# Optimization experiments

Measured on AMD Instinct MI355X. Metric: run time of the kernel, lower is better.

## Reference

```python
import jax, jax.numpy as jnp
import numpy as np

B, S, D_IN, D_OUT = 4, 4096, 1024, 1024

def setup_inputs() -> dict:
    key = jax.random.key(0)
    kx, kq, kk, kv = jax.random.split(key, 4)
    x = jax.random.normal(kx, (B, S, D_IN), dtype=jnp.float32)
    # torch nn.Linear stores weight as [d_out, d_in]; y = x @ W.T
    Wq = jax.random.normal(kq, (D_OUT, D_IN), dtype=jnp.float32) * 0.02
    Wk = jax.random.normal(kk, (D_OUT, D_IN), dtype=jnp.float32) * 0.02
    Wv = jax.random.normal(kv, (D_OUT, D_IN), dtype=jnp.float32) * 0.02
    return {"x": x, "Wq": Wq, "Wk": Wk, "Wv": Wv}

def reference(x, Wq, Wk, Wv):
    b, n, _ = x.shape
    d_out = Wk.shape[0]
    q = jnp.einsum('bnd,od->bno', x, Wq)
    k = jnp.einsum('bnd,od->bno', x, Wk)
    v = jnp.einsum('bnd,od->bno', x, Wv)
    scores = jnp.einsum('bqo,bko->bqk', q, k)  # [B, S, S]
    causal = jnp.triu(jnp.ones((n, n), dtype=bool), k=1)
    scores = jnp.where(causal, -jnp.inf, scores)
    attn = jax.nn.softmax(scores / jnp.sqrt(jnp.float32(d_out)), axis=-1)
    # dropout p=0.0 -> identity
    return jnp.einsum('bqk,bko->bqo', attn, v)
```

## Files before the change

### kernel.cpp

```cpp
#include <hip/hip_runtime.h>


typedef unsigned short u16;
typedef unsigned int u32;
typedef __attribute__((ext_vector_type(8))) short bf16x8;
typedef __attribute__((ext_vector_type(4))) float f32x4;
typedef __attribute__((ext_vector_type(8))) unsigned short u16x8;

__device__ __forceinline__ u16 f2bf(float f) {
  union { float f; unsigned u; } v; v.f = f;
  unsigned r = v.u + 0x7FFFu + ((v.u >> 16) & 1u);
  return (u16)(r >> 16);
}
__device__ __forceinline__ float bf2f(u16 h) {
  union { unsigned u; float f; } v; v.u = ((unsigned)h) << 16;
  return v.f;
}
__device__ __forceinline__ f32x4 mfma16(bf16x8 a, bf16x8 b, f32x4 c) {
  return __builtin_amdgcn_mfma_f32_16x16x32_bf16(a, b, c, 0, 0, 0);
}
__device__ __forceinline__ void gld_lds16(const u16* g, u16* l) {
  __builtin_amdgcn_global_load_lds(
      (const __attribute__((address_space(1))) u32*)g,
      (__attribute__((address_space(3))) u32*)l, 16, 0, 0);
}
#define BAR() __builtin_amdgcn_s_barrier()
#define LGKM0() do { asm volatile("s_waitcnt lgkmcnt(0)" ::: "memory"); \
                     __builtin_amdgcn_sched_barrier(0); } while (0)
#define VMCNT2() asm volatile("s_waitcnt vmcnt(2)" ::: "memory")
#define VMCNT0() asm volatile("s_waitcnt vmcnt(0)" ::: "memory")

__global__ __launch_bounds__(256)
void cast_f32_bf16(const float* __restrict__ src, u16* __restrict__ dst, int n8) {
  int i = blockIdx.x * 256 + threadIdx.x;
  if (i >= n8) return;
  const float4* s4 = (const float4*)src;
  float4 a = s4[2*i], b = s4[2*i+1];
  u16x8 o;
  o[0]=f2bf(a.x); o[1]=f2bf(a.y); o[2]=f2bf(a.z); o[3]=f2bf(a.w);
  o[4]=f2bf(b.x); o[5]=f2bf(b.y); o[6]=f2bf(b.z); o[7]=f2bf(b.w);
  ((u16x8*)dst)[i] = o;
}

#define GEMM8_CORE(Abase, Bbase)                                              \
  auto stageA = [&](int bufi, int h, int t) {                                 \
    _Pragma("unroll")                                                         \
    for (int i = 0; i < 2; ++i) {                                             \
      int ci = i * 512 + tid;                                                 \
      int r  = ci >> 3;                                                       \
      int c  = (ci & 7) ^ (r & 7);                                            \
      gld_lds16(Abase + (size_t)(h * 128 + r) * 1024 + t * 64 + c * 8,        \
                &At[bufi][h][ci * 8]);                                        \
    }                                                                         \
  };                                                                          \
  auto stageB = [&](int bufi, int h, int t) {                                 \
    _Pragma("unroll")                                                         \
    for (int i = 0; i < 2; ++i) {                                             \
      int ci = i * 512 + tid;                                                 \
      int r  = ci >> 3;                                                       \
      int c  = (ci & 7) ^ (r & 7);                                            \
      gld_lds16(Bbase + (size_t)(h * 128 + r) * 1024 + t * 64 + c * 8,        \
                &Bt[bufi][h][ci * 8]);                                        \
    }                                                                         \
  };                                                                          \
  bf16x8 af[4][2], bfr[2][2];                                                 \
  auto readA = [&](int bufi, int mb) {                                        \
    _Pragma("unroll")                                                         \
    for (int m = 0; m < 4; ++m)                                               \
      _Pragma("unroll")                                                       \
      for (int dk = 0; dk < 2; ++dk) {                                        \
        int r  = (mb + m) * 16 + c16;                                         \
        int ch = dk * 4 + g;                                                  \
        af[m][dk] = *(const bf16x8*)&At[bufi][wr][r * 64 + ((ch ^ (r & 7)) * 8)]; \
      }                                                                       \
  };                                                                          \
  auto readB = [&](int bufi, int nb) {                                        \
    _Pragma("unroll")                                                         \
    for (int n = 0; n < 2; ++n)                                               \
      _Pragma("unroll")                                                       \
      for (int dk = 0; dk < 2; ++dk) {                                        \
        int r  = (wc & 1) * 64 + (nb + n) * 16 + c16;                         \
        int ch = dk * 4 + g;                                                  \
        bfr[n][dk] = *(const bf16x8*)&Bt[bufi][wc >> 1][r * 64 + ((ch ^ (r & 7)) * 8)]; \
      }                                                                       \
  };                                                                          \
  auto domfma = [&](int mb, int nb) {                                         \
    __builtin_amdgcn_s_setprio(1);                                            \
    _Pragma("unroll")                                                         \
    for (int dk = 0; dk < 2; ++dk)                                            \
      _Pragma("unroll")                                                       \
      for (int m = 0; m < 4; ++m)                                             \
        _Pragma("unroll")                                                     \
        for (int n = 0; n < 2; ++n)                                           \
          acc[mb + m][nb + n] = mfma16(af[m][dk], bfr[n][dk], acc[mb + m][nb + n]); \
    __builtin_amdgcn_s_setprio(0);                                            \
  };                                                                          \
                \
  stageB(0, 0, 0); stageB(0, 1, 0); stageA(0, 0, 0); stageA(0, 1, 0);         \
  stageB(1, 0, 1);                                                            \
  VMCNT2();                                                                   \
  BAR();                                                                      \
  for (int it = 0; it < 8; ++it) {                                            \
    const bool pf = (it < 7);                                                 \
    const int t1 = 2 * it + 1, t2 = 2 * it + 2, t3 = 2 * it + 3;              \
                                               \
    readA(0, 0); readB(0, 0);                                                 \
    stageB(1, 1, t1);                                                         \
    BAR(); LGKM0();                                                           \
    domfma(0, 0);                                                             \
    BAR();                                                                    \
                                                    \
    readA(0, 4);                                                              \
    stageA(1, 0, t1);                                                         \
    BAR(); LGKM0();                                                           \
    domfma(4, 0);                                                             \
    BAR();                                                                    \
                                                    \
    readB(0, 2);                                                              \
    stageA(1, 1, t1);                                                         \
    BAR(); LGKM0();                                                           \
    domfma(4, 2);                                                             \
    BAR();                                                                    \
                                    \
    readA(0, 0);                                                              \
    if (pf) stageB(0, 0, t2);                                                 \
    BAR(); LGKM0();                                                           \
    domfma(0, 2);                                                             \
    if (pf) { VMCNT2(); } else { VMCNT0(); }                                  \
    BAR();                                                                    \
                                                             \
    readA(1, 0); readB(1, 0);                                                 \
    if (pf) stageB(0, 1, t2);                                                 \
    BAR(); LGKM0();                                                           \
    domfma(0, 0);                                                             \
    BAR();                                                                    \
                                                                  \
    readA(1, 4);                                                              \
    if (pf) stageA(0, 0, t2);                                                 \
    BAR(); LGKM0();                                                           \
    domfma(4, 0);                                                             \
    BAR();                                                                    \
                                                                  \
    readB(1, 2);                                                              \
    if (pf) stageA(0, 1, t2);                                                 \
    BAR(); LGKM0();                                                           \
    domfma(4, 2);                                                             \
    BAR();                                                                    \
                                                  \
    readA(1, 0);                                                              \
    if (pf) stageB(1, 0, t3);                                                 \
    BAR(); LGKM0();                                                           \
    domfma(0, 2);                                                             \
    if (pf) { VMCNT2(); } else { VMCNT0(); }                                  \
    BAR();                                                                    \
  }

__global__ __launch_bounds__(512, 1)
void qkv_gemm(const u16* __restrict__ X, const u16* __restrict__ W,
              u16* __restrict__ Qo, u16* __restrict__ Ko, u16* __restrict__ VTo) {
  __shared__ __align__(16) u16 At[2][2][128 * 64];
  __shared__ __align__(16) u16 Bt[2][2][128 * 64];
  const int tid = threadIdx.x;
  const int w = tid >> 6, lane = tid & 63;
  const int g = lane >> 4, c16 = lane & 15;
  const int wr = w >> 2, wc = w & 3;
  const int M0 = blockIdx.x * 256;
  const int N0 = blockIdx.y * 256;
  const u16* Abase = X + (size_t)M0 * 1024;
  const u16* Bbase = W + (size_t)N0 * 1024;

  f32x4 acc[8][4] = {};
  GEMM8_CORE(Abase, Bbase);

  const int which = N0 >> 10;
  const int colbase = N0 & 1023;
#pragma unroll
  for (int m = 0; m < 8; ++m) {
#pragma unroll
    for (int n = 0; n < 4; ++n) {
#pragma unroll
      for (int r = 0; r < 4; ++r) {
        int gm  = M0 + wr * 128 + m * 16 + 4 * g + r;
        int col = colbase + wc * 64 + n * 16 + c16;
        u16 hv = f2bf(acc[m][n][r]);
        if (which == 0) {
          Qo[(size_t)gm * 1024 + col] = hv;
        } else if (which == 1) {
          Ko[(size_t)gm * 1024 + col] = hv;
        } else {
          int b = gm >> 12, s2 = gm & 4095;
          VTo[((size_t)((b << 10) + col)) * 4096 + s2] = hv;
        }
      }
    }
  }
}

__global__ __launch_bounds__(512, 1)
void sgemm_exp(const u16* __restrict__ Q, const u16* __restrict__ K,
               u16* __restrict__ Spack, float* __restrict__ lpart) {
  __shared__ __align__(16) u16 At[2][2][128 * 64];
  __shared__ __align__(16) u16 Bt[2][2][128 * 64];
  __shared__ float lsum[256][4];
  const int tid = threadIdx.x;
  const int w = tid >> 6, lane = tid & 63;
  const int g = lane >> 4, c16 = lane & 15;
  const int wr = w >> 2, wc = w & 3;
  const int b = blockIdx.y;

  int L = blockIdx.x, qt = 0;
  while ((qt + 1) * (qt + 2) / 2 <= L) ++qt;
  const int kt = L - qt * (qt + 1) / 2;

  const u16* Abase = Q + (size_t)b * 4096 * 1024 + (size_t)qt * 256 * 1024;
  const u16* Bbase = K + (size_t)b * 4096 * 1024 + (size_t)kt * 256 * 1024;

  f32x4 acc[8][4] = {};
  GEMM8_CORE(Abase, Bbase);

  const int qt128 = 2 * qt + wr;
  const int kt128 = 2 * kt + (wc >> 1);
  const bool exists = (kt128 <= qt128);
  u16* Sb = Spack + (((size_t)b * 528 + (size_t)(qt128 * (qt128 + 1)) / 2 + kt128) << 14);
  const int q0 = qt * 256, k0g = kt * 256;
  float psum[8][4];
#pragma unroll
  for (int m = 0; m < 8; ++m)
#pragma unroll
    for (int r = 0; r < 4; ++r) psum[m][r] = 0.f;
#pragma unroll
  for (int m = 0; m < 8; ++m) {
#pragma unroll
    for (int n = 0; n < 4; ++n) {
#pragma unroll
      for (int r = 0; r < 4; ++r) {
        int rl = wr * 128 + m * 16 + 4 * g + r;
        int cl = wc * 64 + n * 16 + c16;
        float s = acc[m][n][r] * 0.03125f;
        float p = (k0g + cl <= q0 + rl) ? __expf(s) : 0.f;
        u16 pb = f2bf(p);
        if (exists) Sb[(rl & 127) * 128 + (cl & 127)] = pb;
        psum[m][r] += bf2f(pb);
      }
    }
  }
#pragma unroll
  for (int m = 0; m < 8; ++m)
#pragma unroll
    for (int r = 0; r < 4; ++r) {
      float v = psum[m][r];
      v += __shfl_xor(v, 1, 64);
      v += __shfl_xor(v, 2, 64);
      v += __shfl_xor(v, 4, 64);
      v += __shfl_xor(v, 8, 64);
      psum[m][r] = v;
    }
  if (c16 == 0) {
#pragma unroll
    for (int m = 0; m < 8; ++m)
#pragma unroll
      for (int r = 0; r < 4; ++r)
        lsum[wr * 128 + m * 16 + 4 * g + r][wc] = psum[m][r];
  }
  __syncthreads();
  if (tid < 256) {
    float v = lsum[tid][0] + lsum[tid][1] + lsum[tid][2] + lsum[tid][3];
    lpart[((size_t)b * 4096 + q0 + tid) * 16 + kt] = v;
  }
}

__global__ __launch_bounds__(256)
void lreduce(const float* __restrict__ lpart, float* __restrict__ linv) {
  int row = blockIdx.x * 256 + threadIdx.x;
  int nt  = ((row & 4095) >> 8) + 1;
  const float* p = lpart + (size_t)row * 16;
  float s = 0.f;
  for (int i = 0; i < nt; ++i) s += p[i];
  linv[row] = 1.f / s;
}

__global__ __launch_bounds__(512)
void pv_gemm(const u16* __restrict__ Spack, const u16* __restrict__ VT,
             const u16* __restrict__ ztile, const float* __restrict__ linv,
             float* __restrict__ Out) {
  __shared__ __align__(16) u16 At[2][256 * 64];
  __shared__ __align__(16) u16 Bt[2][128 * 64];
  const int tid = threadIdx.x;
  const int w = tid >> 6, lane = tid & 63;
  const int g = lane >> 4, c16 = lane & 15;
  const int wm = w >> 1, wn = w & 1;
  const int pp = blockIdx.x;
  const int d0 = blockIdx.y;
  const int b  = blockIdx.z;

  const u16* Sp_b = Spack + (size_t)b * 528 * 16384;
  const u16* VTb  = VT + (size_t)b * 1024 * 4096;
  float* Ob = Out + (size_t)b * 4096 * 1024;

  for (int pass = 0; pass < 2; ++pass) {
    const int QT = pass == 0 ? pp : 15 - pp;
    const int M0 = QT * 256;
    const int nsteps = (QT + 1) * 4;
    const int tLo = 2 * QT;
    const size_t triLo = (size_t)(tLo * (tLo + 1)) / 2;
    const size_t triHi = (size_t)((tLo + 1) * (tLo + 2)) / 2;

    f32x4 acc[4][4] = {};

    auto stage = [&](int s, int tt) {
      const int kv0 = tt * 64;
      const int kt128 = tt >> 1;
      const int koff = (tt & 1) * 64;
      const u16* baseLo = (kt128 <= tLo) ? Sp_b + ((triLo + kt128) << 14) : ztile;
      const u16* baseHi = Sp_b + ((triHi + kt128) << 14);
#pragma unroll
      for (int i = 0; i < 4; ++i) {
        int ci = i * 512 + tid;
        int r = ci >> 3;
        int c = (ci & 7) ^ (r & 7);
        const u16* base = (i < 2) ? baseLo : baseHi;
        gld_lds16(base + (size_t)(r & 127) * 128 + koff + c * 8, &At[s][ci * 8]);
      }
#pragma unroll
      for (int i = 0; i < 2; ++i) {
        int ci = i * 512 + tid;
        int r = ci >> 3;
        int c = (ci & 7) ^ (r & 7);
        gld_lds16(VTb + (size_t)(d0 * 128 + r) * 4096 + kv0 + c * 8, &Bt[s][ci * 8]);
      }
    };
    auto compute = [&](int s) {
#pragma unroll
      for (int dk = 0; dk < 2; ++dk) {
        bf16x8 af2[4], bf2[4];
#pragma unroll
        for (int m = 0; m < 4; ++m) {
          int row = wm * 64 + m * 16 + c16;
          int ch = dk * 4 + g;
          af2[m] = *(const bf16x8*)&At[s][row * 64 + ((ch ^ (row & 7)) * 8)];
        }
#pragma unroll
        for (int n = 0; n < 4; ++n) {
          int row = wn * 64 + n * 16 + c16;
          int ch = dk * 4 + g;
          bf2[n] = *(const bf16x8*)&Bt[s][row * 64 + ((ch ^ (row & 7)) * 8)];
        }
#pragma unroll
        for (int m = 0; m < 4; ++m)
#pragma unroll
          for (int n = 0; n < 4; ++n)
            acc[m][n] = mfma16(af2[m], bf2[n], acc[m][n]);
      }
    };

    stage(0, 0);
    __syncthreads();
    int cur = 0;
    for (int t = 0; t < nsteps; ++t) {
      if (t + 1 < nsteps) stage(cur ^ 1, t + 1);
      compute(cur);
      __syncthreads();
      cur ^= 1;
    }

    const float* lb = linv + (size_t)b * 4096 + M0;
#pragma unroll
    for (int m = 0; m < 4; ++m) {
#pragma unroll
      for (int r = 0; r < 4; ++r) {
        int rl = wm * 64 + m * 16 + 4 * g + r;
        float li = lb[rl];
#pragma unroll
        for (int n = 0; n < 4; ++n) {
          int dcol = d0 * 128 + wn * 64 + n * 16 + c16;
          Ob[(size_t)(M0 + rl) * 1024 + dcol] = acc[m][n][r] * li;
        }
      }
    }
  }
}

__global__ __launch_bounds__(512, 2)
void attn_kernel(const u16* __restrict__ Q, const u16* __restrict__ K,
                 const u16* __restrict__ VT, float* __restrict__ Out) {
  __shared__ u16 kv_lds[32 * 1024];
  __shared__ float s_part[4][32][33];
  __shared__ u16 p_lds[32 * 40];
  __shared__ float l_lds[32];

  const int tid = threadIdx.x;
  const int w = tid >> 6, lane = tid & 63;
  const int g = lane >> 4, c16 = lane & 15;
  const int b  = blockIdx.x & 3;
  const int qb = 127 - (blockIdx.x >> 2);
  const int qs = qb * 32;
  const int kh = w & 1, dq = w >> 1;

  const u16* Qb  = Q  + (size_t)b * 4096 * 1024;
  const u16* Kb  = K  + (size_t)b * 4096 * 1024;
  const u16* VTb = VT + (size_t)b * 1024 * 4096;

  bf16x8 qfrag[2][8];
#pragma unroll
  for (int qh = 0; qh < 2; ++qh)
#pragma unroll
    for (int dk = 0; dk < 8; ++dk)
      qfrag[qh][dk] = *(const bf16x8*)(Qb + (size_t)(qs + qh * 16 + c16) * 1024
                                       + dq * 256 + dk * 32 + g * 8);

  f32x4 oacc[2][8] = {};
  if (tid < 32) l_lds[tid] = 0.f;

  const int qrow_p = tid >> 4;
  const int kk     = tid & 15;
  const int gq     = qs + qrow_p;

  for (int j = 0; j <= qb; ++j) {
    const int kv0 = j * 32;
    __syncthreads();
    uint4 rk[8];
#pragma unroll
    for (int i = 0; i < 8; ++i) {
      int ci = i * 512 + tid;
      int r  = ci >> 7;
      int c  = (ci & 127) ^ (r & 7);
      rk[i] = *(const uint4*)(Kb + (size_t)(kv0 + r) * 1024 + c * 8);
    }
#pragma unroll
    for (int i = 0; i < 8; ++i)
      *(uint4*)&kv_lds[(size_t)(i * 512 + tid) * 8] = rk[i];
    __syncthreads();
    f32x4 sacc[2] = {};
#pragma unroll
    for (int dk = 0; dk < 8; ++dk) {
      int kvrow = kh * 16 + c16;
      int ch    = dq * 32 + dk * 4 + g;
      bf16x8 kf = *(const bf16x8*)&kv_lds[kvrow * 1024 + ((ch ^ (kvrow & 7)) * 8)];
      sacc[0] = mfma16(qfrag[0][dk], kf, sacc[0]);
      sacc[1] = mfma16(qfrag[1][dk], kf, sacc[1]);
    }
#pragma unroll
    for (int qh = 0; qh < 2; ++qh)
#pragma unroll
      for (int r = 0; r < 4; ++r)
        s_part[dq][qh * 16 + 4 * g + r][kh * 16 + c16] = sacc[qh][r];
    __syncthreads();
    uint4 rv[8];
#pragma unroll
    for (int i = 0; i < 8; ++i) {
      int ci = i * 512 + tid;
      int d  = ((ci >> 6) << 4) + (ci & 15);
      int c  = (ci >> 4) & 3;
      rv[i] = *(const uint4*)(VTb + (size_t)d * 4096 + kv0 + c * 8);
    }
    {
      float psum = 0.f;
#pragma unroll
      for (int h = 0; h < 2; ++h) {
        int kcol = kk + h * 16;
        float s = s_part[0][qrow_p][kcol] + s_part[1][qrow_p][kcol]
                + s_part[2][qrow_p][kcol] + s_part[3][qrow_p][kcol];
        s *= 0.03125f;
        float p = (kv0 + kcol <= gq) ? __expf(s) : 0.f;
        u16 pb = f2bf(p);
        p_lds[qrow_p * 40 + kcol] = pb;
        psum += bf2f(pb);
      }
#pragma unroll
      for (int off = 1; off < 16; off <<= 1)
        psum += __shfl_xor(psum, off, 64);
      if (kk == 0) l_lds[qrow_p] += psum;
    }
#pragma unroll
    for (int i = 0; i < 8; ++i)
      *(uint4*)&kv_lds[(size_t)(i * 512 + tid) * 8] = rv[i];
    __syncthreads();
    bf16x8 pa0 = *(const bf16x8*)&p_lds[(0  + c16) * 40 + g * 8];
    bf16x8 pa1 = *(const bf16x8*)&p_lds[(16 + c16) * 40 + g * 8];
#pragma unroll
    for (int f = 0; f < 8; ++f) {
      int dcol = w * 128 + f * 16 + c16;
      int pos  = (dcol >> 4) * 64 + g * 16 + (dcol & 15);
      bf16x8 vf = *(const bf16x8*)&kv_lds[(size_t)pos * 8];
      oacc[0][f] = mfma16(pa0, vf, oacc[0][f]);
      oacc[1][f] = mfma16(pa1, vf, oacc[1][f]);
    }
  }

  float* Ob = Out + (size_t)b * 4096 * 1024;
#pragma unroll
  for (int qh = 0; qh < 2; ++qh) {
#pragma unroll
    for (int r = 0; r < 4; ++r) {
      int ql = qh * 16 + 4 * g + r;
      float linvv = 1.f / l_lds[ql];
#pragma unroll
      for (int f = 0; f < 8; ++f)
        Ob[(size_t)(qs + ql) * 1024 + w * 128 + f * 16 + c16] = oacc[qh][f][r] * linvv;
    }
  }
}

extern "C" void kernel_launch(void* const* d_in, const int* in_sizes, int n_in,
                              void* d_out, int out_size, void* d_ws, size_t ws_size,
                              hipStream_t stream) {
  const float* x  = (const float*)d_in[0];
  const float* Wq = (const float*)d_in[1];
  const float* Wk = (const float*)d_in[2];
  const float* Wv = (const float*)d_in[3];
  float* out = (float*)d_out;

  u16* ws    = (u16*)d_ws;
  u16* wWqkv = ws;
  u16* wX    = wWqkv + (size_t)3 * 1024 * 1024;
  u16* wQ    = wX + (size_t)16384 * 1024;
  u16* wK    = wQ + (size_t)16384 * 1024;
  u16* wVT   = wK + (size_t)16384 * 1024;
  u16* wSp   = wVT + (size_t)16384 * 1024;
  float* lpart = (float*)(ws + (size_t)104857600);
  float* linv  = (float*)(ws + (size_t)105906176);

  cast_f32_bf16<<<dim3(8192), 256, 0, stream>>>(x, wX, 16777216 / 8);
  cast_f32_bf16<<<dim3(512), 256, 0, stream>>>(Wq, wWqkv,                 1048576 / 8);
  cast_f32_bf16<<<dim3(512), 256, 0, stream>>>(Wk, wWqkv + 1048576,       1048576 / 8);
  cast_f32_bf16<<<dim3(512), 256, 0, stream>>>(Wv, wWqkv + 2 * 1048576,   1048576 / 8);

  qkv_gemm<<<dim3(64, 12), 512, 0, stream>>>(wX, wWqkv, wQ, wK, wVT);

  if (ws_size >= (size_t)211877888) {
    hipMemsetAsync(wX, 0, 32768, stream);
    sgemm_exp<<<dim3(136, 4), 512, 0, stream>>>(wQ, wK, wSp, lpart);
    lreduce<<<dim3(64), 256, 0, stream>>>(lpart, linv);
    pv_gemm<<<dim3(8, 8, 4), 512, 0, stream>>>(wSp, wVT, wX, linv, out);
  } else {
    attn_kernel<<<dim3(512), 512, 0, stream>>>(wQ, wK, wVT, out);
  }
}
```

Baseline: 398.7 us.

## Fuse cast and lreduce kernels, deepen GEMM prefetch, and remap blocks for XCD locality

Merges the four f32-to-bf16 cast launches into one kernel and folds the row-sum reciprocal reduction into pv_gemm, which now computes it into LDS. This removes several kernel launches and one global round trip. The QKV GEMM core is restructured to keep full A/B fragments in registers and to prefetch a whole k-tile pair ahead, waiting with vmcnt(8). This costs more registers in exchange for less reloading and more loads in flight. Block indices in qkv_gemm and sgemm_exp are remapped so neighbouring tiles land on the same XCD, aiming for better L2 reuse.

```diff
diff --git a/kernel.cpp b/kernel.cpp
--- a/kernel.cpp
+++ b/kernel.cpp
@@ -24,22 +24,29 @@
       (const __attribute__((address_space(1))) u32*)g,
       (__attribute__((address_space(3))) u32*)l, 16, 0, 0);
 }
-#define BAR() __builtin_amdgcn_s_barrier()
+#define BAR() do { __builtin_amdgcn_s_barrier(); \
+                   __builtin_amdgcn_sched_barrier(0); } while (0)
 #define LGKM0() do { asm volatile("s_waitcnt lgkmcnt(0)" ::: "memory"); \
                      __builtin_amdgcn_sched_barrier(0); } while (0)
-#define VMCNT2() asm volatile("s_waitcnt vmcnt(2)" ::: "memory")
-#define VMCNT0() asm volatile("s_waitcnt vmcnt(0)" ::: "memory")
+#define VMC(n) asm volatile("s_waitcnt vmcnt(" #n ")" ::: "memory")
 
 __global__ __launch_bounds__(256)
-void cast_f32_bf16(const float* __restrict__ src, u16* __restrict__ dst, int n8) {
+void cast_all(const float* __restrict__ x, const float* __restrict__ Wq,
+              const float* __restrict__ Wk, const float* __restrict__ Wv,
+              u16* __restrict__ wX, u16* __restrict__ wWqkv) {
   int i = blockIdx.x * 256 + threadIdx.x;
-  if (i >= n8) return;
+  const float* src; u16* dst; int j;
+  if (i < 2097152)        { src = x;  dst = wX;                j = i; }
+  else if (i < 2228224)   { src = Wq; dst = wWqkv;             j = i - 2097152; }
+  else if (i < 2359296)   { src = Wk; dst = wWqkv + 1048576;   j = i - 2228224; }
+  else if (i < 2490368)   { src = Wv; dst = wWqkv + 2097152;   j = i - 2359296; }
+  else return;
   const float4* s4 = (const float4*)src;
-  float4 a = s4[2*i], b = s4[2*i+1];
+  float4 a = s4[2*j], b = s4[2*j+1];
   u16x8 o;
   o[0]=f2bf(a.x); o[1]=f2bf(a.y); o[2]=f2bf(a.z); o[3]=f2bf(a.w);
   o[4]=f2bf(b.x); o[5]=f2bf(b.y); o[6]=f2bf(b.z); o[7]=f2bf(b.w);
-  ((u16x8*)dst)[i] = o;
+  ((u16x8*)dst)[j] = o;
 }
 
 #define GEMM8_CORE(Abase, Bbase)                                              \
@@ -63,7 +70,7 @@
                 &Bt[bufi][h][ci * 8]);                                        \
     }                                                                         \
   };                                                                          \
-  bf16x8 af[4][2], bfr[2][2];                                                 \
+  bf16x8 af[8][2], bfr[4][2];                                                 \
   auto readA = [&](int bufi, int mb) {                                        \
     _Pragma("unroll")                                                         \
     for (int m = 0; m < 4; ++m)                                               \
@@ -71,7 +78,8 @@
       for (int dk = 0; dk < 2; ++dk) {                                        \
         int r  = (mb + m) * 16 + c16;                                         \
         int ch = dk * 4 + g;                                                  \
-        af[m][dk] = *(const bf16x8*)&At[bufi][wr][r * 64 + ((ch ^ (r & 7)) * 8)]; \
+        af[mb + m][dk] =                                                      \
+            *(const bf16x8*)&At[bufi][wr][r * 64 + ((ch ^ (r & 7)) * 8)];     \
       }                                                                       \
   };                                                                          \
   auto readB = [&](int bufi, int nb) {                                        \
@@ -81,7 +89,8 @@
       for (int dk = 0; dk < 2; ++dk) {                                        \
         int r  = (wc & 1) * 64 + (nb + n) * 16 + c16;                         \
         int ch = dk * 4 + g;                                                  \
-        bfr[n][dk] = *(const bf16x8*)&Bt[bufi][wc >> 1][r * 64 + ((ch ^ (r & 7)) * 8)]; \
+        bfr[nb + n][dk] =                                                     \
+            *(const bf16x8*)&Bt[bufi][wc >> 1][r * 64 + ((ch ^ (r & 7)) * 8)];\
       }                                                                       \
   };                                                                          \
   auto domfma = [&](int mb, int nb) {                                         \
@@ -92,66 +101,58 @@
       for (int m = 0; m < 4; ++m)                                             \
         _Pragma("unroll")                                                     \
         for (int n = 0; n < 2; ++n)                                           \
-          acc[mb + m][nb + n] = mfma16(af[m][dk], bfr[n][dk], acc[mb + m][nb + n]); \
+          acc[mb + m][nb + n] =                                               \
+              mfma16(af[mb + m][dk], bfr[nb + n][dk], acc[mb + m][nb + n]);   \
     __builtin_amdgcn_s_setprio(0);                                            \
   };                                                                          \
-                \
-  stageB(0, 0, 0); stageB(0, 1, 0); stageA(0, 0, 0); stageA(0, 1, 0);         \
-  stageB(1, 0, 1);                                                            \
-  VMCNT2();                                                                   \
+                   \
+  stageA(0, 0, 0); stageA(0, 1, 0); stageB(0, 0, 0); stageB(0, 1, 0);         \
+  stageA(1, 0, 1); stageA(1, 1, 1); stageB(1, 0, 1); stageB(1, 1, 1);         \
+  VMC(8);                                         \
   BAR();                                                                      \
   for (int it = 0; it < 8; ++it) {                                            \
     const bool pf = (it < 7);                                                 \
-    const int t1 = 2 * it + 1, t2 = 2 * it + 2, t3 = 2 * it + 3;              \
-                                               \
+    const int t2 = 2 * it + 2, t3 = 2 * it + 3;                               \
+                                   \
     readA(0, 0); readB(0, 0);                                                 \
-    stageB(1, 1, t1);                                                         \
     BAR(); LGKM0();                                                           \
     domfma(0, 0);                                                             \
     BAR();                                                                    \
-                                                    \
+                                   \
     readA(0, 4);                                                              \
-    stageA(1, 0, t1);                                                         \
     BAR(); LGKM0();                                                           \
     domfma(4, 0);                                                             \
     BAR();                                                                    \
-                                                    \
+                     \
     readB(0, 2);                                                              \
-    stageA(1, 1, t1);                                                         \
+    if (pf) { stageA(0, 0, t2); stageA(0, 1, t2); }                           \
     BAR(); LGKM0();                                                           \
     domfma(4, 2);                                                             \
     BAR();                                                                    \
-                                    \
-    readA(0, 0);                                                              \
-    if (pf) stageB(0, 0, t2);                                                 \
-    BAR(); LGKM0();                                                           \
+                         \
+    if (pf) { stageB(0, 0, t2); stageB(0, 1, t2); }                           \
+    BAR();                                                                    \
     domfma(0, 2);                                                             \
-    if (pf) { VMCNT2(); } else { VMCNT0(); }                                  \
-    BAR();                                                                    \
-                                                             \
+    if (pf) { VMC(8); } else { VMC(0); }                                      \
+    BAR();                                                                    \
+                                                   \
     readA(1, 0); readB(1, 0);                                                 \
-    if (pf) stageB(0, 1, t2);                                                 \
     BAR(); LGKM0();                                                           \
     domfma(0, 0);                                                             \
     BAR();                                                                    \
-                                                                  \
     readA(1, 4);                                                              \
-    if (pf) stageA(0, 0, t2);                                                 \
     BAR(); LGKM0();                                                           \
     domfma(4, 0);                                                             \
     BAR();                                                                    \
-                                                                  \
     readB(1, 2);                                                              \
-    if (pf) stageA(0, 1, t2);                                                 \
+    if (pf) { stageA(1, 0, t3); stageA(1, 1, t3); }                           \
     BAR(); LGKM0();                                                           \
     domfma(4, 2);                                                             \
     BAR();                                                                    \
-                                                  \
-    readA(1, 0);                                                              \
-    if (pf) stageB(1, 0, t3);                                                 \
-    BAR(); LGKM0();                                                           \
+    if (pf) { stageB(1, 0, t3); stageB(1, 1, t3); }                           \
+    BAR();                                                                    \
     domfma(0, 2);                                                             \
-    if (pf) { VMCNT2(); } else { VMCNT0(); }                                  \
+    if (pf) { VMC(8); } else { VMC(0); }                                      \
     BAR();                                                                    \
   }
 
@@ -164,8 +165,10 @@
   const int w = tid >> 6, lane = tid & 63;
   const int g = lane >> 4, c16 = lane & 15;
   const int wr = w >> 2, wc = w & 3;
-  const int M0 = blockIdx.x * 256;
-  const int N0 = blockIdx.y * 256;
+  const int lid = blockIdx.x;
+  const int xcd = lid & 7, gg = lid >> 3;
+  const int M0 = ((xcd << 3) | (gg & 7)) * 256;
+  const int N0 = (gg >> 3) * 256;
   const u16* Abase = X + (size_t)M0 * 1024;
   const u16* Bbase = W + (size_t)N0 * 1024;
 
@@ -208,7 +211,8 @@
   const int wr = w >> 2, wc = w & 3;
   const int b = blockIdx.y;
 
-  int L = blockIdx.x, qt = 0;
+  int L = (blockIdx.x & 7) * 17 + (blockIdx.x >> 3);
+  int qt = 0;
   while ((qt + 1) * (qt + 2) / 2 <= L) ++qt;
   const int kt = L - qt * (qt + 1) / 2;
 
@@ -269,22 +273,13 @@
   }
 }
 
-__global__ __launch_bounds__(256)
-void lreduce(const float* __restrict__ lpart, float* __restrict__ linv) {
-  int row = blockIdx.x * 256 + threadIdx.x;
-  int nt  = ((row & 4095) >> 8) + 1;
-  const float* p = lpart + (size_t)row * 16;
-  float s = 0.f;
-  for (int i = 0; i < nt; ++i) s += p[i];
-  linv[row] = 1.f / s;
-}
-
 __global__ __launch_bounds__(512)
 void pv_gemm(const u16* __restrict__ Spack, const u16* __restrict__ VT,
-             const u16* __restrict__ ztile, const float* __restrict__ linv,
+             const u16* __restrict__ ztile, const float* __restrict__ lpart,
              float* __restrict__ Out) {
   __shared__ __align__(16) u16 At[2][256 * 64];
   __shared__ __align__(16) u16 Bt[2][128 * 64];
+  __shared__ float linv_lds[512];
   const int tid = threadIdx.x;
   const int w = tid >> 6, lane = tid & 63;
   const int g = lane >> 4, c16 = lane & 15;
@@ -296,6 +291,16 @@
   const u16* Sp_b = Spack + (size_t)b * 528 * 16384;
   const u16* VTb  = VT + (size_t)b * 1024 * 4096;
   float* Ob = Out + (size_t)b * 4096 * 1024;
+
+  {
+    const int QTr = (tid < 256) ? pp : (15 - pp);
+    const int row = QTr * 256 + (tid & 255);
+    const int nt  = QTr + 1;
+    const float* p = lpart + ((size_t)b * 4096 + row) * 16;
+    float s = 0.f;
+    for (int i = 0; i < nt; ++i) s += p[i];
+    linv_lds[tid] = 1.f / s;
+  }
 
   for (int pass = 0; pass < 2; ++pass) {
     const int QT = pass == 0 ? pp : 15 - pp;
@@ -363,7 +368,7 @@
       cur ^= 1;
     }
 
-    const float* lb = linv + (size_t)b * 4096 + M0;
+    const float* lb = linv_lds + pass * 256;
 #pragma unroll
     for (int m = 0; m < 4; ++m) {
 #pragma unroll
@@ -518,20 +523,15 @@
   u16* wVT   = wK + (size_t)16384 * 1024;
   u16* wSp   = wVT + (size_t)16384 * 1024;
   float* lpart = (float*)(ws + (size_t)104857600);
-  float* linv  = (float*)(ws + (size_t)105906176);
-
-  cast_f32_bf16<<<dim3(8192), 256, 0, stream>>>(x, wX, 16777216 / 8);
-  cast_f32_bf16<<<dim3(512), 256, 0, stream>>>(Wq, wWqkv,                 1048576 / 8);
-  cast_f32_bf16<<<dim3(512), 256, 0, stream>>>(Wk, wWqkv + 1048576,       1048576 / 8);
-  cast_f32_bf16<<<dim3(512), 256, 0, stream>>>(Wv, wWqkv + 2 * 1048576,   1048576 / 8);
-
-  qkv_gemm<<<dim3(64, 12), 512, 0, stream>>>(wX, wWqkv, wQ, wK, wVT);
+
+  cast_all<<<dim3(9728), 256, 0, stream>>>(x, Wq, Wk, Wv, wX, wWqkv);
+
+  qkv_gemm<<<dim3(768), 512, 0, stream>>>(wX, wWqkv, wQ, wK, wVT);
 
   if (ws_size >= (size_t)211877888) {
     hipMemsetAsync(wX, 0, 32768, stream);
     sgemm_exp<<<dim3(136, 4), 512, 0, stream>>>(wQ, wK, wSp, lpart);
-    lreduce<<<dim3(64), 256, 0, stream>>>(lpart, linv);
-    pv_gemm<<<dim3(8, 8, 4), 512, 0, stream>>>(wSp, wVT, wX, linv, out);
+    pv_gemm<<<dim3(8, 8, 4), 512, 0, stream>>>(wSp, wVT, wX, lpart, out);
   } else {
     attn_kernel<<<dim3(512), 512, 0, stream>>>(wQ, wK, wVT, out);
   }
```

Measured after the change: 368.0 us. 1.08x faster.
